# Performance work log

Hardware: AMD Instinct MI355X
Metric: run time of the kernel (lower is better)

## Reference

```python
import jax, jax.numpy as jnp
import numpy as np

B, N, C_IN, C_EMB, G = 16, 1024, 16, 64, 128
NEG = -1e12


def _lap(m):
    # m @ D^-1/2, transpose, @ D^-1/2  (matches torch code incl. transpose)
    d = jnp.sum(m, axis=1) ** -0.5
    return (m * d[None, :]).T * d[None, :]


def setup_inputs():
    key = jax.random.key(0)
    ks = jax.random.split(key, 16)
    f = jax.random.normal
    return {
        'x': f(ks[0], (B, C_IN, N), jnp.float32),
        'ct': f(ks[1], (B, C_EMB, N), jnp.float32),
        'graph_data': jax.random.uniform(ks[2], (2, N, N), dtype=jnp.float32),
        'emb_w': f(ks[3], (C_EMB, C_IN)) / np.sqrt(C_IN).astype(np.float32),
        'emb_b': f(ks[4], (C_EMB,)) * 0.01,
        'emb2_w': f(ks[5], (N, N)) / np.sqrt(N).astype(np.float32),
        'emb2_b': f(ks[6], (N,)) * 0.01,
        'att_W': f(ks[7], (C_EMB, C_EMB)) / np.sqrt(C_EMB).astype(np.float32),
        'att_a': f(ks[8], (2 * C_EMB, 1)) / np.sqrt(2 * C_EMB).astype(np.float32),
        'att_GL': f(ks[9], (N, G)) / np.sqrt(G).astype(np.float32),
        'uai_w': f(ks[10], (C_EMB, C_EMB)) / np.sqrt(C_EMB).astype(np.float32),
        'uai_b': f(ks[11], (C_EMB,)) * 0.01,
        'lin1_w': f(ks[12], (C_EMB, C_EMB)) / np.sqrt(C_EMB).astype(np.float32),
        'lin2_w': f(ks[13], (C_EMB, C_EMB)) / np.sqrt(C_EMB).astype(np.float32),
        'lin2_b': f(ks[14], (C_EMB,)) * 0.01,
        'ln_w': jnp.ones((C_EMB, N), jnp.float32),
        'ln_b': jnp.zeros((C_EMB, N), jnp.float32),
    }


def reference(x, ct, graph_data, emb_w, emb_b, emb2_w, emb2_b, att_W, att_a,
              att_GL, uai_w, uai_b, lin1_w, lin2_w, lin2_b, ln_w, ln_b):
    # emb: Conv1d k=1 -> leaky_relu -> Linear over node axis N
    h0 = jax.nn.leaky_relu(jnp.einsum('bcn,ec->ben', x, emb_w) + emb_b[None, :, None])
    h0 = jnp.einsum('ben,mn->bem', h0, emb2_w) + emb2_b[None, None, :]
    inp = jnp.swapaxes(h0, 1, 2)  # [B,N,C']

    # InterpositionAttention (repeat/cat factorized: e_ij = leakyrelu(a1.h_i + a2.h_j))
    eye = jnp.eye(N, dtype=x.dtype)
    adj_att = jax.nn.softmax(jax.nn.relu(att_GL @ att_GL.T), axis=-1) + eye
    h = inp @ att_W  # [B,N,C']
    e = jax.nn.leaky_relu((h @ att_a[:C_EMB]) + jnp.swapaxes(h @ att_a[C_EMB:], 1, 2))  # [B,N,N]
    att = jax.nn.softmax(jnp.where(adj_att > 0, e, NEG), axis=2)
    x_att = jnp.swapaxes(jax.nn.relu(att @ h), 1, 2)  # [B,C',N]

    # UAI module (eval mode: dropout off -> all MC samples equal -> sigma = 0)
    mu = jnp.swapaxes(x_att, 1, 2) @ uai_w.T + uai_b  # [B,N,C']
    x_uai = jnp.swapaxes(mu, 1, 2)  # [B,C',N]

    g1 = _lap(graph_data[0] + eye)
    g2 = _lap(graph_data[1] + eye)

    # learned adjacency from pairwise squared distances (cdist p=2, squared)
    xf = jnp.swapaxes(x_uai, 1, 2)  # [B,N,C']
    sq = jnp.sum(xf * xf, axis=-1)
    d2 = jnp.maximum(sq[:, :, None] + sq[:, None, :] - 2.0 * (xf @ jnp.swapaxes(xf, 1, 2)), 0.0)
    gl = jax.nn.softmax(jnp.exp(-d2 / (2.0 * C_EMB)) + eye, axis=-1)  # sigma^2 = emb_size

    def ln(z):  # LayerNorm over last two dims [C', N]
        m = jnp.mean(z, axis=(1, 2), keepdims=True)
        v = jnp.var(z, axis=(1, 2), keepdims=True)
        return (z - m) / jnp.sqrt(v + 1e-5) * ln_w + ln_b

    l1 = lambda z: jnp.einsum('oc,bcn->bon', lin1_w, z)
    l2 = lambda z: jnp.einsum('oc,bcn->bon', lin2_w, z) + lin2_b[None, :, None]

    x_new = ln(l1(x_uai) @ gl + l1(l1(x_uai) @ g1) @ g2)
    ft = jax.nn.gelu(ln(l2(x_uai) @ gl + l2(l2(x_uai) @ g1) @ g2), approximate=False)
    rt = ft  # rt is computed by the identical expression (dropout off)

    ct_new = ft * ct + x_new - ft * x_new
    ht = rt * jax.nn.elu(ct_new) + x_uai - rt * x_uai
    return (ht, ct_new)
```

## Files before the change

### kernel.cpp

```cpp
#include <hip/hip_runtime.h>
#include <math.h>

typedef unsigned short u16;
typedef __attribute__((ext_vector_type(8))) short short8;
typedef __attribute__((ext_vector_type(4))) float floatx4;

constexpr int BATCH = 16;
constexpr int NI = 1024;
constexpr int CE = 64;
constexpr int CI = 16;
constexpr long long NN2  = (long long)NI * NI;
constexpr long long BCN  = (long long)BATCH * CE * NI;
constexpr long long BNv  = (long long)BATCH * NI;
constexpr long long BNN  = (long long)BATCH * NI * NI;
constexpr long long S1 = (long long)CE * NI;
constexpr long long S2 = 2 * S1;
constexpr int ZERON = (int)(2 * BNv + 80);

__device__ __forceinline__ float lrelu01(float x) { return x > 0.f ? x : 0.01f * x; }

__device__ __forceinline__ u16 f2bf(float f) {
  unsigned u = __builtin_bit_cast(unsigned, f);
  return (u16)((u + 0x7fffu + ((u >> 16) & 1u)) >> 16);
}
__device__ __forceinline__ float bf2f(u16 h) {
  unsigned u = ((unsigned)h) << 16;
  return __builtin_bit_cast(float, u);
}
__device__ __forceinline__ unsigned fkey(float f) {
  unsigned u = __builtin_bit_cast(unsigned, f);
  return (u & 0x80000000u) ? ~u : (u | 0x80000000u);
}
__device__ __forceinline__ float funkey(unsigned k) {
  unsigned u = (k & 0x80000000u) ? (k & 0x7fffffffu) : ~k;
  return __builtin_bit_cast(float, u);
}

__device__ __forceinline__ void gload16(const u16* g, u16* l) {
  __builtin_amdgcn_global_load_lds(
      (const __attribute__((address_space(1))) void*)g,
      (__attribute__((address_space(3))) void*)l, 16, 0, 0);
}

template<int BM, int BN, int MODE>
__global__ __launch_bounds__(256) void mgemm(
    const u16* __restrict__ Ag, const u16* __restrict__ B1g, const u16* __restrict__ B2g,
    int K1, int K, int lda, int ldb, long long bsA, long long bsB1,
    float* __restrict__ Cf, u16* __restrict__ Cb, int ldc, long long bsC,
    const float* __restrict__ aux1, const float* __restrict__ aux2,
    const float* __restrict__ aux3, const float* __restrict__ aux4,
    float* __restrict__ Zout)
{
  constexpr int RM = BM / 2, RN = BN / 2, MI = RM / 16, NJ = RN / 16;
  __shared__ __align__(16) u16 As[BM * 64];
  __shared__ __align__(16) u16 Bs[BN * 64];
  __shared__ __align__(16) u16 xa[MODE == 13 ? 32 * 72 : 1];
  const int tid = threadIdx.x;
  int z, n0, r0;
  if constexpr (MODE == 15) {
    const int id = blockIdx.x;
    if (id >= 512) {
      const int m = id - 512;
      float s = 0.f, sv = 0.f;
      for (int n = tid; n < NI; n += 256) {
        float g = aux3[(long long)m * NI + n] * aux2[n];
        s += g;
        sv = fmaf(g, aux1[n], sv);
      }
      float* r1 = (float*)As;
      float* r2 = (float*)As + 256;
      r1[tid] = s; r2[tid] = sv; __syncthreads();
      for (int st = 128; st > 0; st >>= 1) {
        if (tid < st) { r1[tid] += r1[tid + st]; r2[tid] += r2[tid + st]; }
        __syncthreads();
      }
      if (tid == 0) {
        float dm = aux2[m];
        Cf[m] = dm * (r1[0] + dm);
        Zout[m] = dm * (r2[0] + dm * aux1[m]);
      }
      return;
    }
    z = 0; n0 = (id & 15) * BN; r0 = (id >> 4) * BM;
  } else {
    z = blockIdx.z; n0 = blockIdx.x * BN; r0 = blockIdx.y * BM;
  }
  const u16* Ab = Ag + (long long)z * bsA + (long long)r0 * lda;
  const u16* Bb1 = B1g + (long long)z * bsB1 + (long long)n0 * ldb;
  const int lane = tid & 63;
  const int wid = tid >> 6;
  const int wr = wid >> 1, wc = wid & 1;
  const int q = lane >> 4, mlow = lane & 15;
  const int wbase = tid & ~63;

  floatx4 acc[MI][NJ] = {};
  float zp[(BM * 8) / 256] = {};

  for (int k0 = 0; k0 < K; k0 += 64) {
    if constexpr (MODE == 13) {
      const float* s1z = aux2 + (long long)z * NI;
      const float* s2z = aux3 + (long long)z * NI;
      const float mb = funkey(((const unsigned*)aux4)[z]);
#pragma unroll
      for (int s = 0; s < (BM * 8) / 256; s++) {
        int cid = tid + s * 256;
        int r = cid >> 3, craw = cid & 7;
        float s1r = s1z[r0 + r];
        float mr = lrelu01(s1r + mb);
        const float* sp = s2z + k0 + craw * 8;
        float4 sa = *(const float4*)sp;
        float4 sb = *(const float4*)(sp + 4);
        float p0 = __expf(lrelu01(s1r + sa.x) - mr);
        float p1 = __expf(lrelu01(s1r + sa.y) - mr);
        float p2 = __expf(lrelu01(s1r + sa.z) - mr);
        float p3 = __expf(lrelu01(s1r + sa.w) - mr);
        float p4 = __expf(lrelu01(s1r + sb.x) - mr);
        float p5 = __expf(lrelu01(s1r + sb.y) - mr);
        float p6 = __expf(lrelu01(s1r + sb.z) - mr);
        float p7 = __expf(lrelu01(s1r + sb.w) - mr);
        zp[s] += p0 + p1 + p2 + p3 + p4 + p5 + p6 + p7;
        uint4 v;
        v.x = (unsigned)f2bf(p0) | ((unsigned)f2bf(p1) << 16);
        v.y = (unsigned)f2bf(p2) | ((unsigned)f2bf(p3) << 16);
        v.z = (unsigned)f2bf(p4) | ((unsigned)f2bf(p5) << 16);
        v.w = (unsigned)f2bf(p6) | ((unsigned)f2bf(p7) << 16);
        *(uint4*)&As[(r * 8 + (craw ^ (r & 7))) * 8] = v;
      }
    } else {
      const u16* Asrc = Ab + k0;
#pragma unroll
      for (int s = 0; s < (BM * 8) / 256; s++) {
        int cid = tid + s * 256;
        int r = cid >> 3, cc = cid & 7;
        gload16(Asrc + (long long)r * lda + ((cc ^ (r & 7)) << 3),
                As + (((long long)(wbase + s * 256)) << 3));
      }
    }
    {
      const u16* Bsrc = (k0 < K1) ? (Bb1 + k0)
                                  : (B2g + (long long)n0 * ldb + (k0 - K1));
#pragma unroll
      for (int s = 0; s < (BN * 8) / 256; s++) {
        int cid = tid + s * 256;
        int r = cid >> 3, cc = cid & 7;
        gload16(Bsrc + (long long)r * ldb + ((cc ^ (r & 7)) << 3),
                Bs + (((long long)(wbase + s * 256)) << 3));
      }
    }
    __syncthreads();
#pragma unroll
    for (int kh = 0; kh < 2; kh++) {
      const int kc = kh * 4 + q;
      short8 afr[MI], bfr[NJ];
#pragma unroll
      for (int i = 0; i < MI; i++) {
        int row = wr * RM + i * 16 + mlow;
        afr[i] = *(const short8*)&As[(row * 8 + (kc ^ (row & 7))) * 8];
      }
#pragma unroll
      for (int j = 0; j < NJ; j++) {
        int row = wc * RN + j * 16 + mlow;
        bfr[j] = *(const short8*)&Bs[(row * 8 + (kc ^ (row & 7))) * 8];
      }
#pragma unroll
      for (int i = 0; i < MI; i++)
#pragma unroll
        for (int j = 0; j < NJ; j++)
          acc[i][j] = __builtin_amdgcn_mfma_f32_16x16x32_bf16(afr[i], bfr[j], acc[i][j], 0, 0, 0);
    }
    __syncthreads();
  }

  if constexpr (MODE == 3) {
    const float* sqb = aux1 + (long long)z * NI;
#pragma unroll
    for (int i = 0; i < MI; i++) {
#pragma unroll
      for (int rg = 0; rg < 4; rg++) {
        int r = r0 + wr * RM + i * 16 + q * 4 + rg;
        float sqi = sqb[r];
        float rsum = 0.f;
#pragma unroll
        for (int j = 0; j < NJ; j++) {
          int ncol = n0 + wc * RN + j * 16 + mlow;
          float d2 = fmaxf(sqi + sqb[ncol] - 2.f * acc[i][j][rg], 0.f);
          float w = __expf(__expf(-d2 * (1.f / 128.f)) + (r == ncol ? 1.f : 0.f) - 2.f);
          Cb[(long long)z * bsC + (long long)r * ldc + ncol] = f2bf(w);
          rsum += w;
        }
        rsum += __shfl_xor(rsum, 1);
        rsum += __shfl_xor(rsum, 2);
        rsum += __shfl_xor(rsum, 4);
        rsum += __shfl_xor(rsum, 8);
        if (mlow == 0) atomicAdd(&Zout[(long long)z * NI + r], rsum);
      }
    }
  } else if constexpr (MODE == 14) {
    float ps1 = 0.f, ps2 = 0.f;
#pragma unroll
    for (int i = 0; i < MI; i++) {
#pragma unroll
      for (int rg = 0; rg < 4; rg++) {
        int r = wr * RM + i * 16 + q * 4 + rg;
        int ncol = n0 + wc * RN + mlow;
        float v = acc[i][0][rg] + aux3[r] * aux1[ncol];
        Cb[(long long)z * bsC + (long long)r * ldc + ncol] = f2bf(v);
        ps1 = fmaf(v, aux2[r], ps1);
        ps2 = fmaf(v, aux2[64 + r], ps2);
      }
    }
    ps1 += __shfl_xor(ps1, 16); ps1 += __shfl_xor(ps1, 32);
    ps2 += __shfl_xor(ps2, 16); ps2 += __shfl_xor(ps2, 32);
    float* sred = (float*)As;
    const int col = wc * RN + mlow;
    if (q == 0) { sred[col * 2 + wr] = ps1; sred[64 + col * 2 + wr] = ps2; }
    __syncthreads();
    if (tid < 32) {
      float v1 = sred[tid * 2] + sred[tid * 2 + 1];
      float v2 = sred[64 + tid * 2] + sred[64 + tid * 2 + 1];
      Cf[(long long)z * NI + n0 + tid] = v1;
      Zout[(long long)z * NI + n0 + tid] = v2;
      float mx = v2;
      for (int off = 1; off < 32; off <<= 1) mx = fmaxf(mx, __shfl_xor(mx, off));
      if (tid == 0) atomicMax((unsigned*)B2g + z, fkey(mx));
    }
  } else if constexpr (MODE == 13) {
    float* zred = (float*)xa;
    float* zinv = (float*)xa + 256;
    zred[(tid >> 3) * 8 + (tid & 7)] = zp[0];
    __syncthreads();
    if (tid < 32) {
      float sum = 0.f;
#pragma unroll
      for (int j = 0; j < 8; j++) sum += zred[tid * 8 + j];
      zinv[tid] = 1.f / sum;
    }
    __syncthreads();
    float zr[4];
#pragma unroll
    for (int rg = 0; rg < 4; rg++) zr[rg] = zinv[wr * 16 + q * 4 + rg];
    __syncthreads();
#pragma unroll
    for (int j = 0; j < NJ; j++) {
#pragma unroll
      for (int rg = 0; rg < 4; rg++) {
        int row = wr * 16 + q * 4 + rg;
        int col = wc * RN + j * 16 + mlow;
        float v = fmaxf(acc[0][j][rg] * zr[rg], 0.f);
        xa[row * 72 + col] = f2bf(v);
      }
    }
#pragma unroll
    for (int s = 0; s < 2; s++) {
      int cid = tid + s * 256;
      int r = cid >> 3, cc = cid & 7;
      gload16(B2g + r * 64 + ((cc ^ (r & 7)) << 3),
              Bs + (((long long)(wbase + s * 256)) << 3));
    }
    __syncthreads();
    floatx4 acc2[2] = {};
#pragma unroll
    for (int kh = 0; kh < 2; kh++) {
      const int kc = kh * 4 + q;
      short8 a2 = *(const short8*)&xa[(wr * 16 + mlow) * 72 + kc * 8];
#pragma unroll
      for (int j = 0; j < 2; j++) {
        int orow = wc * 32 + j * 16 + mlow;
        short8 b2 = *(const short8*)&Bs[(orow * 8 + (kc ^ (orow & 7))) * 8];
        acc2[j] = __builtin_amdgcn_mfma_f32_16x16x32_bf16(a2, b2, acc2[j], 0, 0, 0);
      }
    }
#pragma unroll
    for (int rg = 0; rg < 4; rg++) {
      int row = r0 + wr * 16 + q * 4 + rg;
      float sqp = 0.f;
#pragma unroll
      for (int j = 0; j < 2; j++) {
        int o = wc * 32 + j * 16 + mlow;
        float v = acc2[j][rg] + aux1[o];
        Cb[(long long)z * bsC + (long long)row * ldc + o] = f2bf(v);
        sqp = fmaf(v, v, sqp);
      }
      sqp += __shfl_xor(sqp, 1);
      sqp += __shfl_xor(sqp, 2);
      sqp += __shfl_xor(sqp, 4);
      sqp += __shfl_xor(sqp, 8);
      if (mlow == 0) atomicAdd(&Zout[(long long)z * NI + row], sqp);
    }
  } else if constexpr (MODE == 5) {
    float ts = 0.f, tss = 0.f;
#pragma unroll
    for (int i = 0; i < MI; i++) {
#pragma unroll
      for (int j = 0; j < NJ; j++) {
#pragma unroll
        for (int rg = 0; rg < 4; rg++) {
          int r = r0 + wr * RM + i * 16 + q * 4 + rg;
          int ncol = n0 + wc * RN + j * 16 + mlow;
          float v = acc[i][j][rg];
          v += aux3[r] * aux1[ncol] + aux4[r] * aux2[ncol];
          Cb[(long long)z * bsC + (long long)r * ldc + ncol] = f2bf(v);
          ts += v;
          tss = fmaf(v, v, tss);
        }
      }
    }
    float* red = (float*)As;
    red[tid] = ts; red[256 + tid] = tss;
    __syncthreads();
    for (int st = 128; st > 0; st >>= 1) {
      if (tid < st) { red[tid] += red[tid + st]; red[256 + tid] += red[256 + tid + st]; }
      __syncthreads();
    }
    if (tid == 0) {
      const int half = r0 >> 6;
      atomicAdd(&Zout[z * 2 + half], red[0]);
      atomicAdd(&Zout[32 + z * 2 + half], red[256]);
    }
  } else {
#pragma unroll
    for (int i = 0; i < MI; i++) {
#pragma unroll
      for (int j = 0; j < NJ; j++) {
#pragma unroll
        for (int rg = 0; rg < 4; rg++) {
          int r = r0 + wr * RM + i * 16 + q * 4 + rg;
          int ncol = n0 + wc * RN + j * 16 + mlow;
          float v = acc[i][j][rg];
          if constexpr (MODE == 4) {
            int blk = r >> 6, oo = r & 63;
            int drow = ((blk & 1) << 6) + oo;
            if (blk < 2) v = (v + aux3[drow]) / aux1[(long long)z * NI + ncol];
            Cb[(long long)z * bsC + (long long)drow * 2048 + (long long)(blk >> 1) * 1024 + ncol] =
                f2bf(v);
          } else {
            Cb[(long long)z * bsC + (long long)r * ldc + ncol] = f2bf(v);
          }
        }
      }
    }
  }
}

__global__ __launch_bounds__(256) void lap_rowsum(const float* __restrict__ gd,
                                                  float* __restrict__ dr,
                                                  float* __restrict__ zero)
{
  if (blockIdx.x >= 2048) {
    int i = (blockIdx.x - 2048) * 256 + threadIdx.x;
    if (i < ZERON) zero[i] = 0.f;
    return;
  }
  const int ki = blockIdx.x;
  const float* row = gd + (long long)ki * NI;
  float s = 0.f;
  for (int j = threadIdx.x; j < NI; j += 256) s += row[j];
  __shared__ float red[256];
  red[threadIdx.x] = s; __syncthreads();
  for (int st = 128; st > 0; st >>= 1) {
    if (threadIdx.x < st) red[threadIdx.x] += red[threadIdx.x + st];
    __syncthreads();
  }
  if (threadIdx.x == 0) dr[ki] = rsqrtf(red[0] + 1.f);
}

__global__ __launch_bounds__(256) void mega_prep(
    const float* __restrict__ l1w, const float* __restrict__ l2w,
    const float* __restrict__ l2b, const float* __restrict__ uaiw,
    const float* __restrict__ attW,
    u16* __restrict__ stack4, float* __restrict__ rb2ext, float* __restrict__ rl2ext,
    u16* __restrict__ uaiw_bf, u16* __restrict__ attwT_bf, float* __restrict__ wcs,
    const float* __restrict__ emb2w, u16* __restrict__ emb2w_bf,
    const float* __restrict__ x, const float* __restrict__ ew,
    const float* __restrict__ eb, u16* __restrict__ h0aT,
    const float* __restrict__ gd, const float* __restrict__ dsum,
    u16* __restrict__ g2t, u16* __restrict__ g1,
    float* __restrict__ cs1)
{
  __shared__ float sm[1092];
  const int bid = blockIdx.x;
  const int t = threadIdx.x;
  if (bid < 98) {
    const int gid = bid * 256 + t;
    if (gid < 4096) {
      stack4[gid] = f2bf(l1w[gid]);
    } else if (gid < 8192) {
      stack4[gid] = f2bf(l2w[gid - 4096]);
    } else if (gid < 12288) {
      int tt = gid - 8192, o = tt >> 6, m = tt & 63;
      float s = 0.f;
      for (int c = 0; c < 64; c++) s = fmaf(l1w[o * 64 + c], l1w[c * 64 + m], s);
      stack4[gid] = f2bf(s);
    } else if (gid < 16384) {
      int tt = gid - 12288, o = tt >> 6, m = tt & 63;
      float s = 0.f;
      for (int c = 0; c < 64; c++) s = fmaf(l2w[o * 64 + c], l2w[c * 64 + m], s);
      stack4[gid] = f2bf(s);
    } else if (gid < 16512) {
      int r = gid - 16384;
      rb2ext[r] = (r < 64) ? 0.f : l2b[r - 64];
    } else if (gid < 16640) {
      int r = gid - 16512;
      float v = 0.f;
      if (r >= 64) { int o = r - 64; for (int c = 0; c < 64; c++) v = fmaf(l2w[o * 64 + c], l2b[c], v); }
      rl2ext[r] = v;
    } else if (gid < 20736) {
      uaiw_bf[gid - 16640] = f2bf(uaiw[gid - 16640]);
    } else if (gid < 24832) {
      int idx = gid - 20736;
      int c = idx >> 6, e = idx & 63;
      attwT_bf[idx] = f2bf(attW[e * 64 + c]);
    } else if (gid < 24896) {
      int c = gid - 24832;
      float s = 0.f;
      for (int e = 0; e < 64; e++) s += attW[e * 64 + c];
      wcs[c] = s;
    }
  } else if (bid < 4194) {
    const long long i = (long long)(bid - 98) * 256 + t;
    emb2w_bf[i] = f2bf(emb2w[i]);
  } else if (bid < 4450) {
    const int sub = bid - 4194;
    const int b = sub >> 4;
    const int nc = (sub & 15) * 64;
    float* we = sm;
    float* be = sm + 1024;
    for (int i = t; i < 1024; i += 256) we[i] = ew[i];
    if (t < 64) be[t] = eb[t];
    __syncthreads();
    const int n = nc + (t >> 2);
    const int e0 = (t & 3) * 16;
    const float* xb = x + (long long)b * CI * NI + n;
    float xv[16];
#pragma unroll
    for (int c = 0; c < CI; c++) xv[c] = xb[(long long)c * NI];
    u16 out16[16];
#pragma unroll
    for (int ee = 0; ee < 16; ee++) {
      const int e = e0 + ee;
      float a = be[e];
#pragma unroll
      for (int c = 0; c < CI; c++) a = fmaf(xv[c], we[e * 16 + c], a);
      out16[ee] = f2bf(lrelu01(a));
    }
    u16* dst = h0aT + (long long)b * S1 + (long long)n * 64 + e0;
    *(uint4*)dst = *(uint4*)out16;
    *(uint4*)(dst + 8) = *(uint4*)(out16 + 8);
  } else if (bid < 8546) {
    const long long idx = (long long)(bid - 4450) * 256 + t;
    const int m = (int)(idx >> 10), j = (int)(idx & 1023);
    const float* d = dsum + NI;
    float v = (gd[NN2 + idx] + (m == j ? 1.f : 0.f)) * d[m] * d[j];
    g2t[idx] = f2bf(v);
  } else if (bid < 9570) {
    const int sub = bid - 8546;
    const int bx = (sub & 31) * 32, by = (sub >> 5) * 32;
    const int lx = t & 31, ly = t >> 5;
    float* tile = sm;
    for (int yy = ly; yy < 32; yy += 8)
      tile[yy * 33 + lx] = gd[(long long)(by + yy) * NI + bx + lx];
    __syncthreads();
    for (int yy = ly; yy < 32; yy += 8) {
      const int i = bx + yy, j = by + lx;
      float v = (tile[lx * 33 + yy] + (i == j ? 1.f : 0.f)) * dsum[i] * dsum[j];
      g1[(long long)i * NI + j] = f2bf(v);
    }
  } else {
    const int n = bid - 9570;
    float s = 0.f;
    for (int i = t; i < NI; i += 256) s = fmaf(gd[(long long)n * NI + i], dsum[i], s);
    float* red = sm;
    red[t] = s; __syncthreads();
    for (int st = 128; st > 0; st >>= 1) {
      if (t < st) red[t] += red[t + st];
      __syncthreads();
    }
    if (t == 0) cs1[n] = dsum[n] * (red[0] + dsum[n]);
  }
}

__global__ __launch_bounds__(256) void ln_final_t(const u16* __restrict__ T,
                                                  const float* __restrict__ stats,
                                                  const float* __restrict__ lnw,
                                                  const float* __restrict__ lnb,
                                                  const float* __restrict__ ct,
                                                  const u16* __restrict__ xuT,
                                                  float* __restrict__ outp)
{
  __shared__ float xs[64 * 65];
  const int blk = blockIdx.x;
  const int b = blk >> 4;
  const int n0 = (blk & 15) << 6;
  const int t = threadIdx.x;
  const int tc = t & 63, tr = t >> 6;
#pragma unroll
  for (int i = 0; i < 16; i++) {
    int nn = i * 4 + tr;
    xs[tc * 65 + nn] = bf2f(xuT[((long long)b << 16) + (long long)(n0 + nn) * 64 + tc]);
  }
  __syncthreads();
  const float inv_n = 1.f / 65536.f;
  const float m0 = stats[b * 2] * inv_n;
  const float m1 = stats[b * 2 + 1] * inv_n;
  const float rs0 = rsqrtf(fmaxf(stats[32 + b * 2] * inv_n - m0 * m0, 0.f) + 1e-5f);
  const float rs1 = rsqrtf(fmaxf(stats[32 + b * 2 + 1] * inv_n - m1 * m1, 0.f) + 1e-5f);
#pragma unroll
  for (int j = 0; j < 16; j++) {
    const int c = j * 4 + tr;
    const int n = n0 + tc;
    const int rem = c * NI + n;
    const long long toff = (long long)b * S2 + rem;
    const float t0 = bf2f(T[toff]);
    const float t1 = bf2f(T[toff + S1]);
    const float w = lnw[rem], bb = lnb[rem];
    const float xn = (t0 - m0) * rs0 * w + bb;
    float ft = (t1 - m1) * rs1 * w + bb;
    ft = 0.5f * ft * (1.f + erff(ft * 0.70710678118654752f));
    const float u = xs[c * 65 + tc];
    const long long oidx = ((long long)b << 16) + rem;
    const float cn = fmaf(ft, ct[oidx] - xn, xn);
    const float el = cn > 0.f ? cn : expm1f(cn);
    outp[oidx] = fmaf(ft, el - u, u);
    outp[BCN + oidx] = cn;
  }
}

extern "C" void kernel_launch(void* const* d_in, const int* in_sizes, int n_in,
                              void* d_out, int out_size, void* d_ws, size_t ws_size,
                              hipStream_t stream)
{
  (void)in_sizes; (void)n_in; (void)out_size; (void)ws_size;
  const float* x      = (const float*)d_in[0];
  const float* ct     = (const float*)d_in[1];
  const float* gdata  = (const float*)d_in[2];
  const float* emb_w  = (const float*)d_in[3];
  const float* emb_b  = (const float*)d_in[4];
  const float* emb2_w = (const float*)d_in[5];
  const float* emb2_b = (const float*)d_in[6];
  const float* att_W  = (const float*)d_in[7];
  const float* att_a  = (const float*)d_in[8];
  const float* uai_w  = (const float*)d_in[10];
  const float* uai_b  = (const float*)d_in[11];
  const float* lin1_w = (const float*)d_in[12];
  const float* lin2_w = (const float*)d_in[13];
  const float* lin2_b = (const float*)d_in[14];
  const float* ln_w   = (const float*)d_in[15];
  const float* ln_b   = (const float*)d_in[16];
  float* outp = (float*)d_out;

  float* ws = (float*)d_ws;
  long long o = 0;
  auto af = [&](long long n) { float* p = ws + o; o += (n + 63) & ~63LL; return p; };
  auto au = [&](long long n) { return (u16*)af((n + 1) / 2); };

  float* s1      = af(BNv);
  float* s2      = af(BNv);
  float* dsum    = af(2 * NI);
  float* cs1v    = af(NI);
  float* cs2v    = af(NI);
  float* v2v     = af(NI);
  float* rb2ext  = af(128);
  float* rl2ext  = af(128);
  float* wcs     = af(64);
  float* zeroreg = af(ZERON);
  float* Zgl     = zeroreg;
  float* sqv     = zeroreg + BNv;
  float* stats   = zeroreg + 2 * BNv;
  unsigned* s2mU = (unsigned*)(stats + 64);
  u16* Tacc      = au(S2 * BATCH);
  u16* emb2w_bf  = au(NN2);
  u16* h0aTb     = au(S1 * BATCH);
  u16* ybf       = au(S1 * BATCH);
  u16* hTb       = au(S1 * BATCH);
  u16* xuaiTb    = au(S1 * BATCH);
  u16* g1b       = au(NN2);
  u16* g2tb      = au(NN2);
  u16* G12b      = au(NN2);
  u16* Abig      = au((long long)BATCH * 128 * 2048);
  u16* stack4    = au(256 * 64);
  u16* uaiw_bf   = au(CE * CE);
  u16* attwT_bf  = au(CE * CE);
  u16* bigW      = au(BNN);

  lap_rowsum<<<2048 + (ZERON + 255) / 256, 256, 0, stream>>>(gdata, dsum, zeroreg);

  mega_prep<<<10594, 256, 0, stream>>>(
      lin1_w, lin2_w, lin2_b, uai_w, att_W,
      stack4, rb2ext, rl2ext, uaiw_bf, attwT_bf, wcs,
      emb2_w, emb2w_bf, x, emb_w, emb_b, h0aTb,
      gdata, dsum, g2tb, g1b, cs1v);

  mgemm<32, 64, 15><<<1536, 256, 0, stream>>>(
      g2tb, g1b, nullptr, NI, NI, NI, NI, 0, 0,
      cs2v, G12b, NI, 0, cs1v, dsum + NI, gdata + NN2, nullptr, v2v);

  mgemm<64, 64, 6><<<dim3(16, 1, BATCH), 256, 0, stream>>>(
      attwT_bf, h0aTb, nullptr, CE, CE, CE, CE, 0, S1,
      nullptr, ybf, NI, S1, nullptr, nullptr, nullptr, nullptr, nullptr);

  mgemm<64, 32, 14><<<dim3(32, 1, BATCH), 256, 0, stream>>>(
      ybf, emb2w_bf, (const u16*)s2mU, NI, NI, NI, NI, S1, 0,
      s1, hTb, NI, S1, emb2_b, att_a, wcs, nullptr, s2);

  mgemm<32, 64, 13><<<dim3(1, 32, BATCH), 256, 0, stream>>>(
      hTb, hTb, uaiw_bf, NI, NI, NI, NI, 0, S1,
      nullptr, xuaiTb, CE, S1, uai_b, s1, s2, (const float*)s2mU, sqv);

  mgemm<128, 128, 3><<<dim3(8, 8, BATCH), 256, 0, stream>>>(
      xuaiTb, xuaiTb, nullptr, CE, CE, CE, CE, S1, S1,
      nullptr, bigW, NI, NN2, sqv, nullptr, nullptr, nullptr, Zgl);

  mgemm<64, 64, 4><<<dim3(16, 4, BATCH), 256, 0, stream>>>(
      stack4, xuaiTb, nullptr, CE, CE, CE, CE, 0, S1,
      nullptr, Abig, 0, (long long)128 * 2048, Zgl, nullptr, rb2ext, nullptr, nullptr);

  mgemm<64, 64, 5><<<dim3(16, 2, BATCH), 256, 0, stream>>>(
      Abig, bigW, G12b, NI, 2 * NI, 2048, NI, (long long)128 * 2048, NN2,
      nullptr, Tacc, NI, S2, cs2v, v2v, rb2ext, rl2ext, stats);

  ln_final_t<<<256, 256, 0, stream>>>(Tacc, stats, ln_w, ln_b, ct, xuaiTb, outp);
}
```

Measured before the change: 241.4 us.

## Double-buffer LDS tiles in selected GEMM modes to overlap loads with MFMA

Adds a two-stage LDS ping-pong pipeline for GEMM modes 5, 13, 14 and 15. The next K-tile's global-to-LDS loads (and, in mode 13, the on-the-fly softmax numerator generation) are issued before computing the current tile, with a single fence per iteration instead of two syncthreads. This targets exposed load latency in the main loop, at the cost of doubled LDS usage, which may lower occupancy. Mode 13's per-row softmax setup is hoisted out of the loop, which assumes BM is 32.

```diff
diff --git a/kernel.cpp b/kernel.cpp
--- a/kernel.cpp
+++ b/kernel.cpp
@@ -42,6 +42,13 @@
       (__attribute__((address_space(3))) void*)l, 16, 0, 0);
 }
 
+__device__ __forceinline__ void pipe_fence() {
+  asm volatile("s_waitcnt vmcnt(0) lgkmcnt(0)" ::: "memory");
+  __builtin_amdgcn_sched_barrier(0);
+  __builtin_amdgcn_s_barrier();
+  __builtin_amdgcn_sched_barrier(0);
+}
+
 template<int BM, int BN, int MODE>
 __global__ __launch_bounds__(256) void mgemm(
     const u16* __restrict__ Ag, const u16* __restrict__ B1g, const u16* __restrict__ B2g,
@@ -52,8 +59,12 @@
     float* __restrict__ Zout)
 {
   constexpr int RM = BM / 2, RN = BN / 2, MI = RM / 16, NJ = RN / 16;
-  __shared__ __align__(16) u16 As[BM * 64];
-  __shared__ __align__(16) u16 Bs[BN * 64];
+  constexpr bool PIPE = (MODE == 5 || MODE == 13 || MODE == 14 || MODE == 15);
+  constexpr int NBUF = PIPE ? 2 : 1;
+  constexpr int NLA = (BM * 8) / 256;
+  constexpr int NLB = (BN * 8) / 256;
+  __shared__ __align__(16) u16 As[NBUF * BM * 64];
+  __shared__ __align__(16) u16 Bs[NBUF * BN * 64];
   __shared__ __align__(16) u16 xa[MODE == 13 ? 32 * 72 : 1];
   const int tid = threadIdx.x;
   int z, n0, r0;
@@ -94,60 +105,63 @@
   const int wbase = tid & ~63;
 
   floatx4 acc[MI][NJ] = {};
-  float zp[(BM * 8) / 256] = {};
-
-  for (int k0 = 0; k0 < K; k0 += 64) {
-    if constexpr (MODE == 13) {
-      const float* s1z = aux2 + (long long)z * NI;
-      const float* s2z = aux3 + (long long)z * NI;
-      const float mb = funkey(((const unsigned*)aux4)[z]);
-#pragma unroll
-      for (int s = 0; s < (BM * 8) / 256; s++) {
-        int cid = tid + s * 256;
-        int r = cid >> 3, craw = cid & 7;
-        float s1r = s1z[r0 + r];
-        float mr = lrelu01(s1r + mb);
-        const float* sp = s2z + k0 + craw * 8;
-        float4 sa = *(const float4*)sp;
-        float4 sb = *(const float4*)(sp + 4);
-        float p0 = __expf(lrelu01(s1r + sa.x) - mr);
-        float p1 = __expf(lrelu01(s1r + sa.y) - mr);
-        float p2 = __expf(lrelu01(s1r + sa.z) - mr);
-        float p3 = __expf(lrelu01(s1r + sa.w) - mr);
-        float p4 = __expf(lrelu01(s1r + sb.x) - mr);
-        float p5 = __expf(lrelu01(s1r + sb.y) - mr);
-        float p6 = __expf(lrelu01(s1r + sb.z) - mr);
-        float p7 = __expf(lrelu01(s1r + sb.w) - mr);
-        zp[s] += p0 + p1 + p2 + p3 + p4 + p5 + p6 + p7;
-        uint4 v;
-        v.x = (unsigned)f2bf(p0) | ((unsigned)f2bf(p1) << 16);
-        v.y = (unsigned)f2bf(p2) | ((unsigned)f2bf(p3) << 16);
-        v.z = (unsigned)f2bf(p4) | ((unsigned)f2bf(p5) << 16);
-        v.w = (unsigned)f2bf(p6) | ((unsigned)f2bf(p7) << 16);
-        *(uint4*)&As[(r * 8 + (craw ^ (r & 7))) * 8] = v;
-      }
-    } else {
+  float zp0 = 0.f;
+
+  float s1r_13 = 0.f, mr_13 = 0.f;
+  const float* s2z_13 = nullptr;
+  if constexpr (MODE == 13) {
+    const float* s1z = aux2 + (long long)z * NI;
+    s2z_13 = aux3 + (long long)z * NI;
+    const float mb = funkey(((const unsigned*)aux4)[z]);
+    s1r_13 = s1z[r0 + (tid >> 3)];
+    mr_13 = lrelu01(s1r_13 + mb);
+  }
+
+  auto stageAB = [&](int buf, int k0) {
+    if constexpr (MODE != 13) {
       const u16* Asrc = Ab + k0;
 #pragma unroll
-      for (int s = 0; s < (BM * 8) / 256; s++) {
+      for (int s = 0; s < NLA; s++) {
         int cid = tid + s * 256;
         int r = cid >> 3, cc = cid & 7;
         gload16(Asrc + (long long)r * lda + ((cc ^ (r & 7)) << 3),
-                As + (((long long)(wbase + s * 256)) << 3));
-      }
-    }
-    {
-      const u16* Bsrc = (k0 < K1) ? (Bb1 + k0)
-                                  : (B2g + (long long)n0 * ldb + (k0 - K1));
-#pragma unroll
-      for (int s = 0; s < (BN * 8) / 256; s++) {
-        int cid = tid + s * 256;
-        int r = cid >> 3, cc = cid & 7;
-        gload16(Bsrc + (long long)r * ldb + ((cc ^ (r & 7)) << 3),
-                Bs + (((long long)(wbase + s * 256)) << 3));
-      }
-    }
-    __syncthreads();
+                As + buf * (BM * 64) + ((wbase + s * 256) << 3));
+      }
+    }
+    const u16* Bsrc = (k0 < K1) ? (Bb1 + k0)
+                                : (B2g + (long long)n0 * ldb + (k0 - K1));
+#pragma unroll
+    for (int s = 0; s < NLB; s++) {
+      int cid = tid + s * 256;
+      int r = cid >> 3, cc = cid & 7;
+      gload16(Bsrc + (long long)r * ldb + ((cc ^ (r & 7)) << 3),
+              Bs + buf * (BN * 64) + ((wbase + s * 256) << 3));
+    }
+  };
+
+  auto agen = [&](int buf, int k0) {
+    int r = tid >> 3, craw = tid & 7;
+    const float* sp = s2z_13 + k0 + craw * 8;
+    float4 sa = *(const float4*)sp;
+    float4 sb = *(const float4*)(sp + 4);
+    float p0 = __expf(lrelu01(s1r_13 + sa.x) - mr_13);
+    float p1 = __expf(lrelu01(s1r_13 + sa.y) - mr_13);
+    float p2 = __expf(lrelu01(s1r_13 + sa.z) - mr_13);
+    float p3 = __expf(lrelu01(s1r_13 + sa.w) - mr_13);
+    float p4 = __expf(lrelu01(s1r_13 + sb.x) - mr_13);
+    float p5 = __expf(lrelu01(s1r_13 + sb.y) - mr_13);
+    float p6 = __expf(lrelu01(s1r_13 + sb.z) - mr_13);
+    float p7 = __expf(lrelu01(s1r_13 + sb.w) - mr_13);
+    zp0 += p0 + p1 + p2 + p3 + p4 + p5 + p6 + p7;
+    uint4 v;
+    v.x = (unsigned)f2bf(p0) | ((unsigned)f2bf(p1) << 16);
+    v.y = (unsigned)f2bf(p2) | ((unsigned)f2bf(p3) << 16);
+    v.z = (unsigned)f2bf(p4) | ((unsigned)f2bf(p5) << 16);
+    v.w = (unsigned)f2bf(p6) | ((unsigned)f2bf(p7) << 16);
+    *(uint4*)&As[buf * (BM * 64) + (r * 8 + (craw ^ (r & 7))) * 8] = v;
+  };
+
+  auto compute_tile = [&](int buf) {
 #pragma unroll
     for (int kh = 0; kh < 2; kh++) {
       const int kc = kh * 4 + q;
@@ -155,12 +169,12 @@
 #pragma unroll
       for (int i = 0; i < MI; i++) {
         int row = wr * RM + i * 16 + mlow;
-        afr[i] = *(const short8*)&As[(row * 8 + (kc ^ (row & 7))) * 8];
+        afr[i] = *(const short8*)&As[buf * (BM * 64) + (row * 8 + (kc ^ (row & 7))) * 8];
       }
 #pragma unroll
       for (int j = 0; j < NJ; j++) {
         int row = wc * RN + j * 16 + mlow;
-        bfr[j] = *(const short8*)&Bs[(row * 8 + (kc ^ (row & 7))) * 8];
+        bfr[j] = *(const short8*)&Bs[buf * (BN * 64) + (row * 8 + (kc ^ (row & 7))) * 8];
       }
 #pragma unroll
       for (int i = 0; i < MI; i++)
@@ -168,7 +182,29 @@
         for (int j = 0; j < NJ; j++)
           acc[i][j] = __builtin_amdgcn_mfma_f32_16x16x32_bf16(afr[i], bfr[j], acc[i][j], 0, 0, 0);
     }
-    __syncthreads();
+  };
+
+  if constexpr (PIPE) {
+    stageAB(0, 0);
+    if constexpr (MODE == 13) agen(0, 0);
+    pipe_fence();
+    int cur = 0;
+    for (int k0 = 0; k0 < K; k0 += 64) {
+      if (k0 + 64 < K) {
+        stageAB(cur ^ 1, k0 + 64);
+        if constexpr (MODE == 13) agen(cur ^ 1, k0 + 64);
+      }
+      compute_tile(cur);
+      pipe_fence();
+      cur ^= 1;
+    }
+  } else {
+    for (int k0 = 0; k0 < K; k0 += 64) {
+      stageAB(0, k0);
+      __syncthreads();
+      compute_tile(0);
+      __syncthreads();
+    }
   }
 
   if constexpr (MODE == 3) {
@@ -227,7 +263,7 @@
   } else if constexpr (MODE == 13) {
     float* zred = (float*)xa;
     float* zinv = (float*)xa + 256;
-    zred[(tid >> 3) * 8 + (tid & 7)] = zp[0];
+    zred[(tid >> 3) * 8 + (tid & 7)] = zp0;
     __syncthreads();
     if (tid < 32) {
       float sum = 0.f;
@@ -255,7 +291,7 @@
       int cid = tid + s * 256;
       int r = cid >> 3, cc = cid & 7;
       gload16(B2g + r * 64 + ((cc ^ (r & 7)) << 3),
-              Bs + (((long long)(wbase + s * 256)) << 3));
+              Bs + ((wbase + s * 256) << 3));
     }
     __syncthreads();
     floatx4 acc2[2] = {};
```

After: 232.4 us. 3.7% less time.
